# Performance work log

Hardware: AMD Instinct MI355X
Metric: run time of the kernel (lower is better)

The kernel has to match this reference:

```python
import jax, jax.numpy as jnp
import numpy as np

B, N, D, H = 1, 4096, 1024, 16
HD = D // H  # head_dim = 64


def setup_inputs() -> dict:
    key = jax.random.key(0)
    ks = jax.random.split(key, 5)
    s = 0.02
    return {
        "x": jax.random.normal(ks[0], (B, N, D), dtype=jnp.float32),
        "Wq": jax.random.normal(ks[1], (D, D), dtype=jnp.float32) * s,
        "Wk": jax.random.normal(ks[2], (D, D), dtype=jnp.float32) * s,
        "Wv": jax.random.normal(ks[3], (D, D), dtype=jnp.float32) * s,
        "Wo": jax.random.normal(ks[4], (D, D), dtype=jnp.float32) * s,
        "bo": jnp.zeros((D,), dtype=jnp.float32),
    }


def reference(x, Wq, Wk, Wv, Wo, bo):
    b, n, d = x.shape
    # QKV projections -> [b, h, n, hd]
    def proj(W):
        return jnp.einsum("bnd,de->bne", x, W).reshape(b, n, H, HD).transpose(0, 2, 1, 3)
    q, k, v = proj(Wq), proj(Wk), proj(Wv)
    # Scores [b, h, n, n] with causal mask (matches masked_fill with triu(diag=1))
    scores = jnp.einsum("bhqd,bhkd->bhqk", q, k)
    causal = jnp.tril(jnp.ones((n, n), dtype=bool))
    scores = jnp.where(causal, scores, -jnp.inf)
    attn = jax.nn.softmax(scores / jnp.sqrt(jnp.float32(HD)), axis=-1)
    # dropout p=0.0 -> identity
    ctx = jnp.einsum("bhqk,bhkd->bhqd", attn, v)
    ctx = ctx.transpose(0, 2, 1, 3).reshape(b, n, d)
    return jnp.einsum("bnd,de->bne", ctx, Wo) + bo
```

## Files before the change

kernel.cpp:

```cpp
#include <hip/hip_runtime.h>


#define N_TOK 4096
#define DMODEL 1024
#define NH 16
#define HDIM 64

typedef __bf16 bf16x8 __attribute__((ext_vector_type(8)));
typedef __bf16 bf16x2v __attribute__((ext_vector_type(2)));
typedef short short4v __attribute__((ext_vector_type(4)));
typedef unsigned int uint2v __attribute__((ext_vector_type(2)));
typedef float f32x4 __attribute__((ext_vector_type(4)));

__device__ __forceinline__ unsigned short f2bf(float f) {
  unsigned u = __builtin_bit_cast(unsigned, f);
  u += 0x7FFFu + ((u >> 16) & 1u);
  return (unsigned short)(u >> 16);
}

__device__ __forceinline__ float bf2f(unsigned short u) {
  unsigned x = (unsigned)u << 16;
  return __builtin_bit_cast(float, x);
}

__device__ __forceinline__ unsigned pack2bf(float f0, float f1) {
  unsigned a = __builtin_bit_cast(unsigned, f0);
  unsigned b = __builtin_bit_cast(unsigned, f1);
  a += 0x7FFFu + ((a >> 16) & 1u);
  b += 0x7FFFu + ((b >> 16) & 1u);
  return (a >> 16) | (b & 0xFFFF0000u);
}

__device__ __forceinline__ unsigned packpk(float f0, float f1) {
#if defined(__HIP_DEVICE_COMPILE__) && __has_builtin(__builtin_amdgcn_cvt_pk_bf16_f32)
  bf16x2v r = __builtin_amdgcn_cvt_pk_bf16_f32(f0, f1);
  return __builtin_bit_cast(unsigned, r);
#else
  return pack2bf(f0, f1);
#endif
}

__device__ __forceinline__ f32x4 mfma16x16x16(short4v a, short4v b, f32x4 c) {
#if defined(__HIP_DEVICE_COMPILE__)
#if __has_builtin(__builtin_amdgcn_mfma_f32_16x16x16bf16_1k)
  return __builtin_amdgcn_mfma_f32_16x16x16bf16_1k(a, b, c, 0, 0, 0);
#else
  asm volatile("v_mfma_f32_16x16x16_bf16 %0, %1, %2, %0\n\ts_nop 7\n\ts_nop 1"
               : "+v"(c) : "v"(a), "v"(b));
  return c;
#endif
#else
  return c;
#endif
}

__device__ __forceinline__ void gll16(const unsigned short* g, unsigned short* l) {
#if defined(__HIP_DEVICE_COMPILE__)
  __builtin_amdgcn_global_load_lds((const __attribute__((address_space(1))) void*)g,
                                   (__attribute__((address_space(3))) void*)l, 16, 0, 0);
#endif
}

__global__ __launch_bounds__(256) void prep_kernel(
    const float* __restrict__ x, unsigned short* __restrict__ xb,
    const float* __restrict__ Wq, const float* __restrict__ Wk,
    const float* __restrict__ Wv, const float* __restrict__ Wo,
    unsigned short* __restrict__ Wqt, unsigned short* __restrict__ Wkt,
    unsigned short* __restrict__ Wvt, unsigned short* __restrict__ Wot) {
  const int bx = blockIdx.x;
  if (bx < 4096) {
    const int i = (bx * 256 + threadIdx.x) * 4;
    float4 v = *(const float4*)(x + i);
    ushort4 o;
    o.x = f2bf(v.x); o.y = f2bf(v.y); o.z = f2bf(v.z); o.w = f2bf(v.w);
    *(ushort4*)(xb + i) = o;
    return;
  }
  __shared__ float t[32][33];
  const int r = bx - 4096;
  const int z = r >> 10, rem = r & 1023;
  const int by = rem >> 5, bxx = rem & 31;
  const float* src;
  unsigned short* dst;
  switch (z) {
    case 0: src = Wq; dst = Wqt; break;
    case 1: src = Wk; dst = Wkt; break;
    case 2: src = Wv; dst = Wvt; break;
    default: src = Wo; dst = Wot; break;
  }
  const int tx = threadIdx.x & 31, ty = threadIdx.x >> 5;
  const int xx = bxx * 32 + tx;
  const int y0 = by * 32;
#pragma unroll
  for (int i = 0; i < 32; i += 8) t[ty + i][tx] = src[(y0 + ty + i) * DMODEL + xx];
  __syncthreads();
  const int ox = by * 32 + tx;
  const int oy0 = bxx * 32;
#pragma unroll
  for (int i = 0; i < 32; i += 8) dst[(oy0 + ty + i) * DMODEL + ox] = f2bf(t[tx][ty + i]);
}

__global__ __launch_bounds__(256) void gemm_qkv_kernel(
    const unsigned short* __restrict__ xb,
    const unsigned short* __restrict__ Wqt, const unsigned short* __restrict__ Wkt,
    const unsigned short* __restrict__ Wvt,
    unsigned short* __restrict__ Qg, unsigned short* __restrict__ Kg,
    unsigned short* __restrict__ Vtg) {
  __shared__ unsigned short As[128 * 32];
  __shared__ unsigned short Bs[128 * 32];
  __shared__ unsigned short Tt[64 * 132];
  const int z = blockIdx.z;
  const unsigned short* Bmat = (z == 0) ? Wqt : ((z == 1) ? Wkt : Wvt);
  const int tid = threadIdx.x, lane = tid & 63, wv = tid >> 6;
  const int quad = lane >> 4, l15 = lane & 15;
  const int wm = wv >> 1, wn = wv & 1;
  const int tm0 = blockIdx.y * 128, tn0 = blockIdx.x * 128;
  const int lrow = lane >> 2, lcol = (lane & 3) * 8;
  const f32x4 zero4 = {0.f, 0.f, 0.f, 0.f};
  f32x4 acc[4][4];
#pragma unroll
  for (int i = 0; i < 4; ++i)
#pragma unroll
    for (int j = 0; j < 4; ++j) acc[i][j] = zero4;

  for (int kb = 0; kb < DMODEL; kb += 32) {
#pragma unroll
    for (int r = 0; r < 2; ++r) {
      const int row0 = r * 64 + wv * 16;
      gll16(&xb[(tm0 + row0 + lrow) * DMODEL + kb + lcol], &As[row0 * 32]);
      gll16(&Bmat[(tn0 + row0 + lrow) * DMODEL + kb + lcol], &Bs[row0 * 32]);
    }
    __syncthreads();
    bf16x8 af[4], bfr[4];
#pragma unroll
    for (int i = 0; i < 4; ++i) {
      af[i]  = *(const bf16x8*)&As[(wm * 64 + i * 16 + l15) * 32 + quad * 8];
      bfr[i] = *(const bf16x8*)&Bs[(wn * 64 + i * 16 + l15) * 32 + quad * 8];
    }
#pragma unroll
    for (int mt = 0; mt < 4; ++mt)
#pragma unroll
      for (int nt = 0; nt < 4; ++nt)
        acc[mt][nt] = __builtin_amdgcn_mfma_f32_16x16x32_bf16(af[mt], bfr[nt], acc[mt][nt], 0, 0, 0);
    __syncthreads();
  }

  const float qs = 0.125f * 1.44269504088896f;
  if (z < 2) {
#pragma unroll
    for (int mt = 0; mt < 4; ++mt)
#pragma unroll
      for (int nt = 0; nt < 4; ++nt)
#pragma unroll
        for (int r = 0; r < 4; ++r) {
          const int row = tm0 + wm * 64 + mt * 16 + quad * 4 + r;
          const int col = tn0 + wn * 64 + nt * 16 + l15;
          const float v = acc[mt][nt][r];
          const int hh = col >> 6, hd = col & 63;
          if (z == 0) Qg[(hh * N_TOK + row) * HDIM + hd] = f2bf(v * qs);
          else        Kg[(hh * N_TOK + row) * HDIM + hd] = f2bf(v);
        }
  } else {
#pragma unroll 1
    for (int p = 0; p < 2; ++p) {
      if (wn == p) {
#pragma unroll
        for (int mt = 0; mt < 4; ++mt)
#pragma unroll
          for (int nt = 0; nt < 4; ++nt) {
            const int c = nt * 16 + l15;
#pragma unroll
            for (int r = 0; r < 4; ++r)
              Tt[c * 132 + wm * 64 + mt * 16 + quad * 4 + r] = f2bf(acc[mt][nt][r]);
          }
      }
      __syncthreads();
      const int c = tid >> 2, seg = tid & 3;
      const int hh = (tn0 + p * 64) >> 6;
      unsigned short* dst = Vtg + hh * (HDIM * N_TOK) + c * N_TOK + tm0 + seg * 32;
      const unsigned short* srcp = &Tt[c * 132 + seg * 32];
#pragma unroll
      for (int j = 0; j < 4; ++j)
        *(uint4*)(dst + j * 8) = *(const uint4*)(srcp + j * 8);
      __syncthreads();
    }
  }
}

#define TRW 68

__device__ static const unsigned char T_TAB[63] = {
    10, 11, 12, 13, 14, 15, 16, 17, 18, 19, 20, 21, 22, 23, 24, 25, 26, 27, 28, 29, 30,
    31, 21, 22, 23, 24, 25, 26, 27, 28, 29, 30, 31,
    9, 20, 31, 8, 19, 30, 7, 18, 29, 6, 17, 28, 5, 16, 27,
    4, 15, 26, 3, 14, 25, 2, 13, 24, 1, 12, 23, 0, 11, 22};
__device__ static const unsigned char G_TAB[63] = {
    0, 0, 0, 0, 0, 0, 0, 0, 0, 0, 0, 0, 0, 0, 0, 0, 0, 0, 0, 0, 0,
    0, 1, 1, 1, 1, 1, 1, 1, 1, 1, 1, 1,
    0, 1, 2, 0, 1, 2, 0, 1, 2, 0, 1, 2, 0, 1, 2,
    0, 1, 2, 0, 1, 2, 0, 1, 2, 0, 1, 2, 0, 1, 2};

__device__ __forceinline__ void stage_kv(
    const unsigned short* __restrict__ Kh, const unsigned short* __restrict__ Vh,
    int kv0, char* buf, int wv, int lane) {
  unsigned short* Ksb = (unsigned short*)buf;
  unsigned short* Vsb = (unsigned short*)(buf + 8192);
  const int r8 = lane >> 3, g = lane & 7;
  const int sw = ((g ^ r8) * 8);
#pragma unroll
  for (int i = 0; i < 2; ++i) {
    const int row = wv * 16 + i * 8;
    gll16(&Kh[(kv0 + row + r8) * HDIM + sw], &Ksb[row * 64]);
    gll16(&Vh[(row + r8) * N_TOK + kv0 + sw], &Vsb[row * 64]);
  }
}

template <bool MASKED>
__device__ __forceinline__ void attn_step(
    int kvs, int qw, int quad, int l15,
    const unsigned short* __restrict__ Ks, const unsigned short* __restrict__ Vs,
    const bf16x8 (&qf)[2][2], f32x4 (&o)[2][4], float (&l_)[2]) {
  const f32x4 zero4 = {0.f, 0.f, 0.f, 0.f};
  const int s = l15 & 7;
  f32x4 c[2][4];
#pragma unroll
  for (int mt = 0; mt < 4; ++mt) {
    const unsigned short* kp = &Ks[(mt * 16 + l15) * 64];
    const int g0 = (quad ^ s) * 8;
    const bf16x8 kf0 = *(const bf16x8*)(kp + g0);
    const bf16x8 kf1 = *(const bf16x8*)(kp + (g0 ^ 32));
#pragma unroll
    for (int qt = 0; qt < 2; ++qt) {
      c[qt][mt] = __builtin_amdgcn_mfma_f32_16x16x32_bf16(kf0, qf[qt][0], zero4, 0, 0, 0);
      c[qt][mt] = __builtin_amdgcn_mfma_f32_16x16x32_bf16(kf1, qf[qt][1], c[qt][mt], 0, 0, 0);
    }
  }
  short4v pb[2][4];
#pragma unroll
  for (int qt = 0; qt < 2; ++qt) {
    const int q = qw + qt * 16 + l15;
    float ls = 0.f;
#pragma unroll
    for (int mt = 0; mt < 4; ++mt) {
      float p[4];
#pragma unroll
      for (int r = 0; r < 4; ++r) {
        float v = c[qt][mt][r];
        if (MASKED) v = ((kvs + mt * 16 + quad * 4 + r) <= q) ? v : -3e38f;
        p[r] = exp2f(v);
      }
      ls += (p[0] + p[1]) + (p[2] + p[3]);
      uint2v w;
      w.x = packpk(p[0], p[1]);
      w.y = packpk(p[2], p[3]);
      pb[qt][mt] = __builtin_bit_cast(short4v, w);
    }
    l_[qt] += ls;
  }
#pragma unroll
  for (int mt = 0; mt < 4; ++mt)
#pragma unroll
    for (int dt = 0; dt < 4; ++dt) {
      const int gv = (((2 * mt + (quad >> 1)) ^ s) * 8) + (quad & 1) * 4;
      const short4v vfx = *(const short4v*)&Vs[(dt * 16 + l15) * 64 + gv];
      o[0][dt] = mfma16x16x16(vfx, pb[0][mt], o[0][dt]);
      o[1][dt] = mfma16x16x16(vfx, pb[1][mt], o[1][dt]);
    }
}

__global__ __launch_bounds__(256, 3) void attn_kernel(
    const unsigned short* __restrict__ Qg, const unsigned short* __restrict__ Kg,
    const unsigned short* __restrict__ Vtg, unsigned short* __restrict__ ctx,
    unsigned short* __restrict__ part_o, float* __restrict__ part_l) {
  __shared__ __align__(16) char smem[34816];
  const int tid = threadIdx.x, lane = tid & 63, wv = tid >> 6;
  const int quad = lane >> 4, l15 = lane & 15;

  const int u = blockIdx.x >> 4;
  const int h = blockIdx.x & 15;
  const int t = T_TAB[u], g = G_TAB[u];
  const int c0 = g * 11;
  const int cend = (c0 + 10 < t) ? (c0 + 10) : t;
  const int mlen = 2 * (cend - c0 + 1);
  const bool multi = (t >= 11);
  const int qb = t * 128, qw = qb + wv * 32;

  const unsigned short* Qh = Qg + h * N_TOK * HDIM;
  const unsigned short* Kh = Kg + h * N_TOK * HDIM;
  const unsigned short* Vh = Vtg + h * HDIM * N_TOK;

  bf16x8 qf[2][2];
#pragma unroll
  for (int qt = 0; qt < 2; ++qt)
#pragma unroll
    for (int hh = 0; hh < 2; ++hh)
      qf[qt][hh] = *(const bf16x8*)&Qh[(qw + qt * 16 + l15) * HDIM + hh * 32 + quad * 8];

  const f32x4 zero4 = {0.f, 0.f, 0.f, 0.f};
  f32x4 o[2][4];
#pragma unroll
  for (int qt = 0; qt < 2; ++qt)
#pragma unroll
    for (int dt = 0; dt < 4; ++dt) o[qt][dt] = zero4;
  float l_[2] = {0.f, 0.f};

  const int kvbase = c0 << 7;
  stage_kv(Kh, Vh, kvbase, smem, wv, lane);
  int cur = 0;
#pragma unroll 1
  for (int mc = 0; mc < mlen; ++mc) {
    const int kv0 = kvbase + mc * 64;
    __syncthreads();
    if (mc + 1 < mlen)
      stage_kv(Kh, Vh, kv0 + 64, smem + (cur ^ 1) * 16384, wv, lane);
    const unsigned short* Ksb = (const unsigned short*)(smem + cur * 16384);
    const unsigned short* Vsb = (const unsigned short*)(smem + cur * 16384 + 8192);
    if (kv0 <= qw + 31) {
      if (kv0 + 63 <= qw)
        attn_step<false>(kv0, qw, quad, l15, Ksb, Vsb, qf, o, l_);
      else
        attn_step<true>(kv0, qw, quad, l15, Ksb, Vsb, qf, o, l_);
    }
    cur ^= 1;
  }
  __syncthreads();

  float* Tr = (float*)(smem + wv * (32 * TRW * 4));
  const int tq = lane >> 1, half = lane & 1;
  if (!multi) {
#pragma unroll
    for (int qt = 0; qt < 2; ++qt) {
      float l = l_[qt];
      l += __shfl_xor(l, 16, 64);
      l += __shfl_xor(l, 32, 64);
      const float inv = 1.0f / l;
#pragma unroll
      for (int dt = 0; dt < 4; ++dt) {
        f32x4 v = o[qt][dt] * inv;
        *(f32x4*)&Tr[(qt * 16 + l15) * TRW + dt * 16 + quad * 4] = v;
      }
    }
    unsigned short* dst = &ctx[(qb + wv * 32 + tq) * DMODEL + h * HDIM + half * 32];
    const float* src = &Tr[tq * TRW + half * 32];
#pragma unroll
    for (int j = 0; j < 4; ++j) {
      const float* s8 = src + j * 8;
      uint4 w;
      w.x = pack2bf(s8[0], s8[1]);
      w.y = pack2bf(s8[2], s8[3]);
      w.z = pack2bf(s8[4], s8[5]);
      w.w = pack2bf(s8[6], s8[7]);
      *(uint4*)(dst + j * 8) = w;
    }
  } else {
    const int slot = (h * 21 + (t - 11)) * 3 + g;
#pragma unroll
    for (int qt = 0; qt < 2; ++qt) {
      float l = l_[qt];
      l += __shfl_xor(l, 16, 64);
      l += __shfl_xor(l, 32, 64);
      if (quad == 0) part_l[slot * 128 + wv * 32 + qt * 16 + l15] = l;
#pragma unroll
      for (int dt = 0; dt < 4; ++dt)
        *(f32x4*)&Tr[(qt * 16 + l15) * TRW + dt * 16 + quad * 4] = o[qt][dt];
    }
    unsigned short* dst = part_o + (size_t)slot * 8192 + (wv * 32 + tq) * 64 + half * 32;
    const float* src = &Tr[tq * TRW + half * 32];
#pragma unroll
    for (int j = 0; j < 4; ++j) {
      const float* s8 = src + j * 8;
      uint4 w;
      w.x = pack2bf(s8[0], s8[1]);
      w.y = pack2bf(s8[2], s8[3]);
      w.z = pack2bf(s8[4], s8[5]);
      w.w = pack2bf(s8[6], s8[7]);
      *(uint4*)(dst + j * 8) = w;
    }
  }
}

__global__ __launch_bounds__(256) void merge_kernel(
    const unsigned short* __restrict__ part_o, const float* __restrict__ part_l,
    unsigned short* __restrict__ ctx) {
  const int b = blockIdx.x;
  const int h = b / 21, tt = b % 21;
  const int t = tt + 11;
  const int ng = t / 11 + 1;
  const int tid = threadIdx.x;
  const int q = tid >> 1, half = tid & 1;
  const int s0 = (h * 21 + tt) * 3;
  float l = 0.f;
  for (int g = 0; g < ng; ++g) l += part_l[(s0 + g) * 128 + q];
  const float inv = 1.0f / l;
  unsigned short* dst = &ctx[(t * 128 + q) * DMODEL + h * HDIM + half * 32];
#pragma unroll
  for (int j = 0; j < 4; ++j) {
    float acc[8] = {0.f, 0.f, 0.f, 0.f, 0.f, 0.f, 0.f, 0.f};
    for (int g = 0; g < ng; ++g) {
      const uint4 w = *(const uint4*)(part_o + (size_t)(s0 + g) * 8192 + q * 64 + half * 32 + j * 8);
      const unsigned short* us = (const unsigned short*)&w;
#pragma unroll
      for (int e = 0; e < 8; ++e) acc[e] += bf2f(us[e]);
    }
    uint4 w;
    w.x = pack2bf(acc[0] * inv, acc[1] * inv);
    w.y = pack2bf(acc[2] * inv, acc[3] * inv);
    w.z = pack2bf(acc[4] * inv, acc[5] * inv);
    w.w = pack2bf(acc[6] * inv, acc[7] * inv);
    *(uint4*)(dst + j * 8) = w;
  }
}

__global__ __launch_bounds__(256) void gemm_out_kernel(
    const unsigned short* __restrict__ ctxb, const unsigned short* __restrict__ Wot,
    const float* __restrict__ bo, float* __restrict__ out) {
  __shared__ unsigned short As[128 * 32];
  __shared__ unsigned short Bs[128 * 32];
  const int tid = threadIdx.x, lane = tid & 63, wv = tid >> 6;
  const int quad = lane >> 4, l15 = lane & 15;
  const int wm = wv >> 1, wn = wv & 1;
  const int tm0 = blockIdx.y * 128, tn0 = blockIdx.x * 128;
  const int lrow = lane >> 2, lcol = (lane & 3) * 8;
  const f32x4 zero4 = {0.f, 0.f, 0.f, 0.f};
  f32x4 acc[4][4];
#pragma unroll
  for (int i = 0; i < 4; ++i)
#pragma unroll
    for (int j = 0; j < 4; ++j) acc[i][j] = zero4;

  for (int kb = 0; kb < DMODEL; kb += 32) {
#pragma unroll
    for (int r = 0; r < 2; ++r) {
      const int row0 = r * 64 + wv * 16;
      gll16(&ctxb[(tm0 + row0 + lrow) * DMODEL + kb + lcol], &As[row0 * 32]);
      gll16(&Wot[(tn0 + row0 + lrow) * DMODEL + kb + lcol], &Bs[row0 * 32]);
    }
    __syncthreads();
    bf16x8 af[4], bfr[4];
#pragma unroll
    for (int i = 0; i < 4; ++i) {
      af[i]  = *(const bf16x8*)&As[(wm * 64 + i * 16 + l15) * 32 + quad * 8];
      bfr[i] = *(const bf16x8*)&Bs[(wn * 64 + i * 16 + l15) * 32 + quad * 8];
    }
#pragma unroll
    for (int mt = 0; mt < 4; ++mt)
#pragma unroll
      for (int nt = 0; nt < 4; ++nt)
        acc[mt][nt] = __builtin_amdgcn_mfma_f32_16x16x32_bf16(af[mt], bfr[nt], acc[mt][nt], 0, 0, 0);
    __syncthreads();
  }
#pragma unroll
  for (int mt = 0; mt < 4; ++mt)
#pragma unroll
    for (int nt = 0; nt < 4; ++nt)
#pragma unroll
      for (int r = 0; r < 4; ++r) {
        const int row = tm0 + wm * 64 + mt * 16 + quad * 4 + r;
        const int col = tn0 + wn * 64 + nt * 16 + l15;
        out[row * DMODEL + col] = acc[mt][nt][r] + bo[col];
      }
}

extern "C" void kernel_launch(void* const* d_in, const int* in_sizes, int n_in,
                              void* d_out, int out_size, void* d_ws, size_t ws_size,
                              hipStream_t stream) {
  const float* x  = (const float*)d_in[0];
  const float* Wq = (const float*)d_in[1];
  const float* Wk = (const float*)d_in[2];
  const float* Wv = (const float*)d_in[3];
  const float* Wo = (const float*)d_in[4];
  const float* bo = (const float*)d_in[5];
  float* out = (float*)d_out;

  char* ws = (char*)d_ws;
  unsigned short* xb  = (unsigned short*)(ws);
  unsigned short* Wqt = (unsigned short*)(ws + 8388608);
  unsigned short* Wkt = (unsigned short*)(ws + 8388608 + 2097152);
  unsigned short* Wvt = (unsigned short*)(ws + 8388608 + 2 * 2097152);
  unsigned short* Wot = (unsigned short*)(ws + 8388608 + 3 * 2097152);
  unsigned short* Qg  = (unsigned short*)(ws + 16777216);
  unsigned short* Kg  = (unsigned short*)(ws + 25165824);
  unsigned short* Vtg = (unsigned short*)(ws + 33554432);
  unsigned short* ctx = xb;
  unsigned short* part_o = (unsigned short*)(ws + 41943040);
  float* part_l = (float*)(ws + 58458112);

  prep_kernel<<<8192, 256, 0, stream>>>(x, xb, Wq, Wk, Wv, Wo, Wqt, Wkt, Wvt, Wot);
  gemm_qkv_kernel<<<dim3(DMODEL / 128, N_TOK / 128, 3), 256, 0, stream>>>(xb, Wqt, Wkt, Wvt, Qg, Kg, Vtg);
  attn_kernel<<<1008, 256, 0, stream>>>(Qg, Kg, Vtg, ctx, part_o, part_l);
  merge_kernel<<<336, 256, 0, stream>>>(part_o, part_l, ctx);
  gemm_out_kernel<<<dim3(DMODEL / 128, N_TOK / 128), 256, 0, stream>>>(ctx, Wot, bo, out);
}
```

Baseline: 235.4 us.

## Split attention block into eight waves of 16 queries with fast exp2

The attention kernel now launches 512 threads (8 waves), and each wave owns 16 query rows instead of 32. This halves per-wave register state (accumulators, Q fragments) and adds waves for latency hiding, and the KV staging work is spread across the extra waves. It also replaces exp2f with the hardware v_exp_f32 intrinsic and raises wave priority around the MFMA compute section. The cost is that each loaded K/V fragment is reused by fewer queries per wave, so LDS reads per MFMA roughly double.

```diff
diff --git a/kernel.cpp b/kernel.cpp
--- a/kernel.cpp
+++ b/kernel.cpp
@@ -37,6 +37,20 @@
   return __builtin_bit_cast(unsigned, r);
 #else
   return pack2bf(f0, f1);
+#endif
+}
+
+__device__ __forceinline__ float fast_exp2(float x) {
+#if defined(__HIP_DEVICE_COMPILE__)
+#if __has_builtin(__builtin_amdgcn_exp2f)
+  return __builtin_amdgcn_exp2f(x);
+#else
+  float r;
+  asm("v_exp_f32 %0, %1" : "=v"(r) : "v"(x));
+  return r;
+#endif
+#else
+  return exp2f(x);
 #endif
 }
 
@@ -207,68 +221,58 @@
   unsigned short* Vsb = (unsigned short*)(buf + 8192);
   const int r8 = lane >> 3, g = lane & 7;
   const int sw = ((g ^ r8) * 8);
-#pragma unroll
-  for (int i = 0; i < 2; ++i) {
-    const int row = wv * 16 + i * 8;
-    gll16(&Kh[(kv0 + row + r8) * HDIM + sw], &Ksb[row * 64]);
-    gll16(&Vh[(row + r8) * N_TOK + kv0 + sw], &Vsb[row * 64]);
-  }
+  const int row = wv * 8;
+  gll16(&Kh[(kv0 + row + r8) * HDIM + sw], &Ksb[row * 64]);
+  gll16(&Vh[(row + r8) * N_TOK + kv0 + sw], &Vsb[row * 64]);
 }
 
 template <bool MASKED>
 __device__ __forceinline__ void attn_step(
     int kvs, int qw, int quad, int l15,
     const unsigned short* __restrict__ Ks, const unsigned short* __restrict__ Vs,
-    const bf16x8 (&qf)[2][2], f32x4 (&o)[2][4], float (&l_)[2]) {
+    const bf16x8 (&qf)[2], f32x4 (&o)[4], float& l_) {
   const f32x4 zero4 = {0.f, 0.f, 0.f, 0.f};
   const int s = l15 & 7;
-  f32x4 c[2][4];
+  const int g0 = (quad ^ s) * 8;
+  f32x4 c[4];
 #pragma unroll
   for (int mt = 0; mt < 4; ++mt) {
     const unsigned short* kp = &Ks[(mt * 16 + l15) * 64];
-    const int g0 = (quad ^ s) * 8;
     const bf16x8 kf0 = *(const bf16x8*)(kp + g0);
     const bf16x8 kf1 = *(const bf16x8*)(kp + (g0 ^ 32));
-#pragma unroll
-    for (int qt = 0; qt < 2; ++qt) {
-      c[qt][mt] = __builtin_amdgcn_mfma_f32_16x16x32_bf16(kf0, qf[qt][0], zero4, 0, 0, 0);
-      c[qt][mt] = __builtin_amdgcn_mfma_f32_16x16x32_bf16(kf1, qf[qt][1], c[qt][mt], 0, 0, 0);
-    }
-  }
-  short4v pb[2][4];
-#pragma unroll
-  for (int qt = 0; qt < 2; ++qt) {
-    const int q = qw + qt * 16 + l15;
-    float ls = 0.f;
-#pragma unroll
-    for (int mt = 0; mt < 4; ++mt) {
-      float p[4];
-#pragma unroll
-      for (int r = 0; r < 4; ++r) {
-        float v = c[qt][mt][r];
-        if (MASKED) v = ((kvs + mt * 16 + quad * 4 + r) <= q) ? v : -3e38f;
-        p[r] = exp2f(v);
-      }
-      ls += (p[0] + p[1]) + (p[2] + p[3]);
-      uint2v w;
-      w.x = packpk(p[0], p[1]);
-      w.y = packpk(p[2], p[3]);
-      pb[qt][mt] = __builtin_bit_cast(short4v, w);
-    }
-    l_[qt] += ls;
-  }
+    c[mt] = __builtin_amdgcn_mfma_f32_16x16x32_bf16(kf0, qf[0], zero4, 0, 0, 0);
+    c[mt] = __builtin_amdgcn_mfma_f32_16x16x32_bf16(kf1, qf[1], c[mt], 0, 0, 0);
+  }
+  short4v pb[4];
+  const int q = qw + l15;
+  float ls = 0.f;
+#pragma unroll
+  for (int mt = 0; mt < 4; ++mt) {
+    float p[4];
+#pragma unroll
+    for (int r = 0; r < 4; ++r) {
+      float v = c[mt][r];
+      if (MASKED) v = ((kvs + mt * 16 + quad * 4 + r) <= q) ? v : -3e38f;
+      p[r] = fast_exp2(v);
+    }
+    ls += (p[0] + p[1]) + (p[2] + p[3]);
+    uint2v w;
+    w.x = packpk(p[0], p[1]);
+    w.y = packpk(p[2], p[3]);
+    pb[mt] = __builtin_bit_cast(short4v, w);
+  }
+  l_ += ls;
 #pragma unroll
   for (int mt = 0; mt < 4; ++mt)
 #pragma unroll
     for (int dt = 0; dt < 4; ++dt) {
       const int gv = (((2 * mt + (quad >> 1)) ^ s) * 8) + (quad & 1) * 4;
       const short4v vfx = *(const short4v*)&Vs[(dt * 16 + l15) * 64 + gv];
-      o[0][dt] = mfma16x16x16(vfx, pb[0][mt], o[0][dt]);
-      o[1][dt] = mfma16x16x16(vfx, pb[1][mt], o[1][dt]);
-    }
-}
-
-__global__ __launch_bounds__(256, 3) void attn_kernel(
+      o[dt] = mfma16x16x16(vfx, pb[mt], o[dt]);
+    }
+}
+
+__global__ __launch_bounds__(512, 8) void attn_kernel(
     const unsigned short* __restrict__ Qg, const unsigned short* __restrict__ Kg,
     const unsigned short* __restrict__ Vtg, unsigned short* __restrict__ ctx,
     unsigned short* __restrict__ part_o, float* __restrict__ part_l) {
@@ -283,26 +287,22 @@
   const int cend = (c0 + 10 < t) ? (c0 + 10) : t;
   const int mlen = 2 * (cend - c0 + 1);
   const bool multi = (t >= 11);
-  const int qb = t * 128, qw = qb + wv * 32;
+  const int qb = t * 128, qw = qb + wv * 16;
 
   const unsigned short* Qh = Qg + h * N_TOK * HDIM;
   const unsigned short* Kh = Kg + h * N_TOK * HDIM;
   const unsigned short* Vh = Vtg + h * HDIM * N_TOK;
 
-  bf16x8 qf[2][2];
-#pragma unroll
-  for (int qt = 0; qt < 2; ++qt)
-#pragma unroll
-    for (int hh = 0; hh < 2; ++hh)
-      qf[qt][hh] = *(const bf16x8*)&Qh[(qw + qt * 16 + l15) * HDIM + hh * 32 + quad * 8];
+  bf16x8 qf[2];
+#pragma unroll
+  for (int hh = 0; hh < 2; ++hh)
+    qf[hh] = *(const bf16x8*)&Qh[(qw + l15) * HDIM + hh * 32 + quad * 8];
 
   const f32x4 zero4 = {0.f, 0.f, 0.f, 0.f};
-  f32x4 o[2][4];
-#pragma unroll
-  for (int qt = 0; qt < 2; ++qt)
-#pragma unroll
-    for (int dt = 0; dt < 4; ++dt) o[qt][dt] = zero4;
-  float l_[2] = {0.f, 0.f};
+  f32x4 o[4];
+#pragma unroll
+  for (int dt = 0; dt < 4; ++dt) o[dt] = zero4;
+  float l_ = 0.f;
 
   const int kvbase = c0 << 7;
   stage_kv(Kh, Vh, kvbase, smem, wv, lane);
@@ -315,35 +315,34 @@
       stage_kv(Kh, Vh, kv0 + 64, smem + (cur ^ 1) * 16384, wv, lane);
     const unsigned short* Ksb = (const unsigned short*)(smem + cur * 16384);
     const unsigned short* Vsb = (const unsigned short*)(smem + cur * 16384 + 8192);
-    if (kv0 <= qw + 31) {
+    if (kv0 <= qw + 15) {
+      __builtin_amdgcn_s_setprio(1);
       if (kv0 + 63 <= qw)
         attn_step<false>(kv0, qw, quad, l15, Ksb, Vsb, qf, o, l_);
       else
         attn_step<true>(kv0, qw, quad, l15, Ksb, Vsb, qf, o, l_);
+      __builtin_amdgcn_s_setprio(0);
     }
     cur ^= 1;
   }
   __syncthreads();
 
-  float* Tr = (float*)(smem + wv * (32 * TRW * 4));
-  const int tq = lane >> 1, half = lane & 1;
+  float* Tr = (float*)(smem + wv * (16 * TRW * 4));
+  const int tq = lane >> 2, seg = lane & 3;
   if (!multi) {
-#pragma unroll
-    for (int qt = 0; qt < 2; ++qt) {
-      float l = l_[qt];
-      l += __shfl_xor(l, 16, 64);
-      l += __shfl_xor(l, 32, 64);
-      const float inv = 1.0f / l;
-#pragma unroll
-      for (int dt = 0; dt < 4; ++dt) {
-        f32x4 v = o[qt][dt] * inv;
-        *(f32x4*)&Tr[(qt * 16 + l15) * TRW + dt * 16 + quad * 4] = v;
-      }
-    }
-    unsigned short* dst = &ctx[(qb + wv * 32 + tq) * DMODEL + h * HDIM + half * 32];
-    const float* src = &Tr[tq * TRW + half * 32];
-#pragma unroll
-    for (int j = 0; j < 4; ++j) {
+    float l = l_;
+    l += __shfl_xor(l, 16, 64);
+    l += __shfl_xor(l, 32, 64);
+    const float inv = 1.0f / l;
+#pragma unroll
+    for (int dt = 0; dt < 4; ++dt) {
+      f32x4 v = o[dt] * inv;
+      *(f32x4*)&Tr[l15 * TRW + dt * 16 + quad * 4] = v;
+    }
+    unsigned short* dst = &ctx[(qb + wv * 16 + tq) * DMODEL + h * HDIM + seg * 16];
+    const float* src = &Tr[tq * TRW + seg * 16];
+#pragma unroll
+    for (int j = 0; j < 2; ++j) {
       const float* s8 = src + j * 8;
       uint4 w;
       w.x = pack2bf(s8[0], s8[1]);
@@ -354,20 +353,17 @@
     }
   } else {
     const int slot = (h * 21 + (t - 11)) * 3 + g;
-#pragma unroll
-    for (int qt = 0; qt < 2; ++qt) {
-      float l = l_[qt];
-      l += __shfl_xor(l, 16, 64);
-      l += __shfl_xor(l, 32, 64);
-      if (quad == 0) part_l[slot * 128 + wv * 32 + qt * 16 + l15] = l;
-#pragma unroll
-      for (int dt = 0; dt < 4; ++dt)
-        *(f32x4*)&Tr[(qt * 16 + l15) * TRW + dt * 16 + quad * 4] = o[qt][dt];
-    }
-    unsigned short* dst = part_o + (size_t)slot * 8192 + (wv * 32 + tq) * 64 + half * 32;
-    const float* src = &Tr[tq * TRW + half * 32];
-#pragma unroll
-    for (int j = 0; j < 4; ++j) {
+    float l = l_;
+    l += __shfl_xor(l, 16, 64);
+    l += __shfl_xor(l, 32, 64);
+    if (quad == 0) part_l[slot * 128 + wv * 16 + l15] = l;
+#pragma unroll
+    for (int dt = 0; dt < 4; ++dt)
+      *(f32x4*)&Tr[l15 * TRW + dt * 16 + quad * 4] = o[dt];
+    unsigned short* dst = part_o + (size_t)slot * 8192 + (wv * 16 + tq) * 64 + seg * 16;
+    const float* src = &Tr[tq * TRW + seg * 16];
+#pragma unroll
+    for (int j = 0; j < 2; ++j) {
       const float* s8 = src + j * 8;
       uint4 w;
       w.x = pack2bf(s8[0], s8[1]);
@@ -487,7 +483,7 @@
 
   prep_kernel<<<8192, 256, 0, stream>>>(x, xb, Wq, Wk, Wv, Wo, Wqt, Wkt, Wvt, Wot);
   gemm_qkv_kernel<<<dim3(DMODEL / 128, N_TOK / 128, 3), 256, 0, stream>>>(xb, Wqt, Wkt, Wvt, Qg, Kg, Vtg);
-  attn_kernel<<<1008, 256, 0, stream>>>(Qg, Kg, Vtg, ctx, part_o, part_l);
+  attn_kernel<<<1008, 512, 0, stream>>>(Qg, Kg, Vtg, ctx, part_o, part_l);
   merge_kernel<<<336, 256, 0, stream>>>(part_o, part_l, ctx);
   gemm_out_kernel<<<dim3(DMODEL / 128, N_TOK / 128), 256, 0, stream>>>(ctx, Wot, bo, out);
 }
```

After: 229.7 us. 1.02x faster.
